# Kernel optimization log

Hardware: AMD Instinct MI355X
Metric: run time of the kernel (lower is better)

## Reference

```python
import jax, jax.numpy as jnp
import numpy as np

PS = 3
B, C, H, W = 4, 256, 64, 64
IMG = 256
_MEAN = np.array([0.485, 0.456, 0.406], dtype=np.float32).reshape(1, 3, 1, 1)
_STD = np.array([0.229, 0.224, 0.225], dtype=np.float32).reshape(1, 3, 1, 1)


def setup_inputs() -> dict:
    key = jax.random.key(0)
    ks = jax.random.split(key, 16)
    d = {
        "dense_features1": jax.random.normal(ks[0], (B, C, H, W), jnp.float32),
        "dense_features2": jax.random.normal(ks[1], (B, C, H, W), jnp.float32),
        "img_ref_hr": jax.random.uniform(ks[2], (B, 3, IMG, IMG), jnp.float32),
        "w1_1": jax.random.normal(ks[3], (64, 3, 3, 3), jnp.float32) * 0.05,
        "b1_1": jnp.zeros((64,), jnp.float32),
        "w1_2": jax.random.normal(ks[4], (64, 64, 3, 3), jnp.float32) * 0.05,
        "b1_2": jnp.zeros((64,), jnp.float32),
        "w2_1": jax.random.normal(ks[5], (128, 64, 3, 3), jnp.float32) * 0.05,
        "b2_1": jnp.zeros((128,), jnp.float32),
        "w2_2": jax.random.normal(ks[6], (128, 128, 3, 3), jnp.float32) * 0.05,
        "b2_2": jnp.zeros((128,), jnp.float32),
        "w3_1": jax.random.normal(ks[7], (256, 128, 3, 3), jnp.float32) * 0.05,
        "b3_1": jnp.zeros((256,), jnp.float32),
    }
    return d


def _conv(x, w, b):
    y = jax.lax.conv_general_dilated(x, w, (1, 1), "SAME",
                                     dimension_numbers=("NCHW", "OIHW", "NCHW"))
    return y + b[None, :, None, None]


def _pool(x):
    return jax.lax.reduce_window(x, -jnp.inf, jax.lax.max, (1, 1, 2, 2), (1, 1, 2, 2), "VALID")


def _vgg(img, w11, b11, w12, b12, w21, b21, w22, b22, w31, b31):
    x = (img - _MEAN) / _STD  # ImageNet input norm (use_input_norm=True)
    r11 = jax.nn.relu(_conv(x, w11, b11))
    x = _pool(jax.nn.relu(_conv(r11, w12, b12)))
    r21 = jax.nn.relu(_conv(x, w21, b21))
    x = _pool(jax.nn.relu(_conv(r21, w22, b22)))
    r31 = jax.nn.relu(_conv(x, w31, b31))
    return r11, r21, r31


def _l2n(f):  # per-pixel channel L2 normalize (F.normalize dim=0, eps=1e-12)
    return f / jnp.maximum(jnp.linalg.norm(f, axis=0, keepdims=True), 1e-12)


def _patches(f):  # (c,h,w) -> (nh*nw, c*PS*PS), row-major patch order
    c, h, w = f.shape
    nh, nw = h - PS + 1, w - PS + 1
    cols = jnp.stack([f[:, i:i + nh, j:j + nw] for i in range(PS) for j in range(PS)], axis=1)
    return cols.reshape(c * PS * PS, nh * nw).T


def _match(fin, fref):
    fin, fref = _l2n(fin), _l2n(fref)
    nh, nw = fin.shape[1] - PS + 1, fin.shape[2] - PS + 1
    p_in = _patches(fin)
    p_ref = _patches(fref)
    p_ref = p_ref / (jnp.linalg.norm(p_ref, axis=1, keepdims=True) + 1e-5)  # is_norm
    corr = p_in @ p_ref.T  # (N_in, N_ref) patch correlation
    return jnp.argmax(corr, axis=1).reshape(nh, nw)


def _index_to_flow(idx):  # (nh,nw) int -> (nh+2, nw+2, 2) float flow
    nh, nw = idx.shape
    fw = (idx % nw).astype(jnp.float32) - jnp.arange(nw, dtype=jnp.float32)[None, :]
    fh = (idx // nw).astype(jnp.float32) - jnp.arange(nh, dtype=jnp.float32)[:, None]
    flow = jnp.stack([fw, fh], axis=-1)
    return jnp.pad(flow, ((0, 2), (0, 2), (0, 0)))


def _shift9(flow, s):  # 9 down/right shifts with zero fill -> (9,H,W,2)
    Hh, Ww, _ = flow.shape
    outs = [jnp.pad(flow, ((i * s, 0), (j * s, 0), (0, 0)))[:Hh, :Ww]
            for i in range(3) for j in range(3)]
    return jnp.stack(outs, axis=0)


def _per_sample(fin, fref):
    flow3 = _index_to_flow(_match(fin, fref))
    off3 = _shift9(flow3, 1)
    flow2 = jnp.repeat(jnp.repeat(flow3, 2, axis=0), 2, axis=1) * 2.0
    off2 = _shift9(flow2, 2)
    flow1 = jnp.repeat(jnp.repeat(flow3, 4, axis=0), 4, axis=1) * 4.0
    off1 = _shift9(flow1, 4)
    return off1, off2, off3


def reference(dense_features1, dense_features2, img_ref_hr,
              w1_1, b1_1, w1_2, b1_2, w2_1, b2_1, w2_2, b2_2, w3_1, b3_1):
    off1, off2, off3 = jax.vmap(_per_sample)(dense_features1, dense_features2)
    r11, r21, r31 = _vgg(img_ref_hr, w1_1, b1_1, w1_2, b1_2, w2_1, b2_1, w2_2, b2_2, w3_1, b3_1)
    # pre_offset['relu1_1'/'relu2_1'/'relu3_1'], img_ref_feat['relu1_1'/'relu2_1'/'relu3_1']
    return (off1, off2, off3, r11, r21, r31)
```

## Files before the change

### kernel.cpp

```cpp
#include <hip/hip_runtime.h>

typedef __attribute__((ext_vector_type(4))) float f32x4;
typedef __attribute__((ext_vector_type(8))) short s16x8;

#define OFF1_OFF 0
#define OFF2_OFF 4718592
#define OFF3_OFF 5898240
#define R11_OFF  6193152
#define R21_OFF  22970368
#define R31_OFF  31358976

__device__ __forceinline__ ushort f2bf(float x) {
  union { float f; uint u; } c; c.f = x;
  uint r = c.u + 0x7FFFu + ((c.u >> 16) & 1u);
  return (ushort)(r >> 16);
}
__device__ __forceinline__ float bfval(ushort h) {
  union { uint u; float f; } c; c.u = ((uint)h) << 16;
  return c.f;
}

__global__ __launch_bounds__(256)
void k_normalize(const float* __restrict__ f1, const float* __restrict__ f2,
                 ushort* __restrict__ n1b, ushort* __restrict__ n2b) {
  __shared__ uint ldsu[64 * 256];
  float* red = (float*)ldsu;
  float* inv = (float*)ldsu + 256;
  const int t = threadIdx.x, x = t & 63, cg = t >> 6;
  const int h = blockIdx.x, b = blockIdx.y;
  const float* in = blockIdx.z ? f2 : f1;
  ushort* op = blockIdx.z ? n2b : n1b;
  const size_t base = (size_t)b * 256 * 4096 + (size_t)h * 64 + x;
  float vals[64];
  float s = 0.f;
  #pragma unroll
  for (int ci = 0; ci < 64; ++ci) {
    float v = in[base + (size_t)(cg * 64 + ci) * 4096];
    vals[ci] = v;
    s = fmaf(v, v, s);
  }
  red[t] = s;
  __syncthreads();
  if (t < 64) {
    float tot = red[t] + red[64 + t] + red[128 + t] + red[192 + t];
    inv[t] = 1.0f / fmaxf(sqrtf(tot), 1e-12f);
  }
  __syncthreads();
  const float iv = inv[x];
  __syncthreads();
  #pragma unroll
  for (int j = 0; j < 32; ++j) {
    float v0 = vals[2 * j] * iv, v1 = vals[2 * j + 1] * iv;
    ushort h0 = f2bf(v0), h1 = f2bf(v1);
    ushort l0 = f2bf(v0 - bfval(h0)), l1 = f2bf(v1 - bfval(h1));
    int cc = (cg << 1) + (j >> 4);
    int i = j & 15;
    int qh = cc * 32 + i, ql = cc * 32 + 16 + i;
    ldsu[x * 256 + (qh ^ (x & 31))] = (uint)h0 | ((uint)h1 << 16);
    ldsu[x * 256 + (ql ^ (x & 31))] = (uint)l0 | ((uint)l1 << 16);
  }
  __syncthreads();
  uint* og = (uint*)(op + ((size_t)b * 4096 + h * 64) * 512);
  #pragma unroll
  for (int it = 0; it < 64; ++it) {
    int idx = it * 256 + t;
    int p = idx >> 8, q = idx & 255;
    og[idx] = ldsu[p * 256 + (q ^ (p & 31))];
  }
}

__global__ __launch_bounds__(256)
void k_pgemm_mfma(const ushort* __restrict__ Ab0, const ushort* __restrict__ Bb0,
                  float* __restrict__ P0) {
  __shared__ __align__(16) ushort As[128 * 64];
  __shared__ __align__(16) ushort Bs[128 * 64];
  const int t = threadIdx.x;
  const int bz = blockIdx.z;
  const ushort* Ab = Ab0 + (size_t)bz * 2097152;
  const ushort* Bb = Bb0 + (size_t)bz * 2097152;
  float* P = P0 + (size_t)bz * 16777216;
  const int u0 = blockIdx.y * 128, v0 = blockIdx.x * 128;
  const int lane = t & 63, wv = t >> 6;
  const int wm = wv >> 1, wn = wv & 1;
  const int lr = lane & 15, lk = lane >> 4;
  int rowv[4], slotv[4];
  #pragma unroll
  for (int i = 0; i < 4; ++i) { int e = t + i * 256; rowv[i] = e >> 3; slotv[i] = e & 7; }
  s16x8 ra[4], rb[4];
  #pragma unroll
  for (int i = 0; i < 4; ++i) {
    ra[i] = *(const s16x8*)(Ab + ((size_t)(u0 + rowv[i])) * 512 + slotv[i] * 8);
    rb[i] = *(const s16x8*)(Bb + ((size_t)(v0 + rowv[i])) * 512 + slotv[i] * 8);
  }
  f32x4 acc[4][4];
  #pragma unroll
  for (int mt = 0; mt < 4; ++mt)
    #pragma unroll
    for (int nt = 0; nt < 4; ++nt) {
      f32x4 z = {0.f, 0.f, 0.f, 0.f};
      acc[mt][nt] = z;
    }

  #pragma unroll 1
  for (int cc = 0; cc < 8; ++cc) {
    __syncthreads();
    #pragma unroll
    for (int i = 0; i < 4; ++i) {
      *(s16x8*)(As + ((rowv[i] << 3) + (slotv[i] ^ (rowv[i] & 7))) * 8) = ra[i];
      *(s16x8*)(Bs + ((rowv[i] << 3) + (slotv[i] ^ (rowv[i] & 7))) * 8) = rb[i];
    }
    __syncthreads();
    if (cc < 7) {
      #pragma unroll
      for (int i = 0; i < 4; ++i) {
        ra[i] = *(const s16x8*)(Ab + ((size_t)(u0 + rowv[i])) * 512 + (cc + 1) * 64 + slotv[i] * 8);
        rb[i] = *(const s16x8*)(Bb + ((size_t)(v0 + rowv[i])) * 512 + (cc + 1) * 64 + slotv[i] * 8);
      }
    }
    s16x8 ah[4], al[4], bh[4], bl[4];
    #pragma unroll
    for (int mt = 0; mt < 4; ++mt) {
      int row = wm * 64 + mt * 16 + lr;
      ah[mt] = *(const s16x8*)(As + ((row << 3) + (lk ^ (row & 7))) * 8);
      al[mt] = *(const s16x8*)(As + ((row << 3) + ((4 + lk) ^ (row & 7))) * 8);
    }
    #pragma unroll
    for (int nt = 0; nt < 4; ++nt) {
      int row = wn * 64 + nt * 16 + lr;
      bh[nt] = *(const s16x8*)(Bs + ((row << 3) + (lk ^ (row & 7))) * 8);
      bl[nt] = *(const s16x8*)(Bs + ((row << 3) + ((4 + lk) ^ (row & 7))) * 8);
    }
    #pragma unroll
    for (int mt = 0; mt < 4; ++mt)
      #pragma unroll
      for (int nt = 0; nt < 4; ++nt) {
        acc[mt][nt] = __builtin_amdgcn_mfma_f32_16x16x32_bf16(al[mt], bh[nt], acc[mt][nt], 0, 0, 0);
        acc[mt][nt] = __builtin_amdgcn_mfma_f32_16x16x32_bf16(ah[mt], bl[nt], acc[mt][nt], 0, 0, 0);
        acc[mt][nt] = __builtin_amdgcn_mfma_f32_16x16x32_bf16(ah[mt], bh[nt], acc[mt][nt], 0, 0, 0);
      }
  }
  const int plane = ((blockIdx.y * 2 + wm) << 6) + blockIdx.x * 2 + wn;
  float* Pp = P + (size_t)plane * 4096;
  #pragma unroll
  for (int mt = 0; mt < 4; ++mt)
    #pragma unroll
    for (int nt = 0; nt < 4; ++nt) {
      #pragma unroll
      for (int r = 0; r < 4; ++r)
        Pp[(mt * 16 + lk * 4 + r) * 64 + nt * 16 + lr] = acc[mt][nt][r];
    }
}

__global__ __launch_bounds__(256)
void k_corr(const float* __restrict__ P0, float* __restrict__ pv0,
            int* __restrict__ pi0) {
  __shared__ __align__(16) f32x4 Pl[3 * 1024];
  __shared__ float rv[256];
  __shared__ int   ri[256];
  const int t = threadIdx.x;
  const int orig = blockIdx.x;
  const int w = (orig & 7) * 1922 + (orig >> 3);
  const int bz = w / 3844;
  const int r2 = w % 3844;
  const int py = r2 / 62, qy = r2 % 62;
  const float* P = P0 + (size_t)bz * 16777216;
  float* pv = pv0 + (size_t)bz * 238328;
  int*   pi = pi0 + (size_t)bz * 238328;
  #pragma unroll
  for (int i = 0; i < 12; ++i) {
    int e = t + i * 256;
    int blk = e >> 10, rem = e & 1023;
    int px = rem >> 4, q4 = rem & 15;
    int pidx = (py + blk) * 64 + (qy + blk);
    f32x4 v = *(const f32x4*)(P + (size_t)pidx * 4096 + rem * 4);
    int slot = ((q4 + (px >> 4)) & 15) ^ (px & 15);
    Pl[blk * 1024 + px * 16 + slot] = v;
  }
  __syncthreads();
  const int px = t & 63, cg = t >> 6;
  #pragma unroll
  for (int j = 0; j < 4; ++j) {
    int c = cg * 4 + j;
    int slot = ((c + (px >> 4)) & 15) ^ (px & 15);
    int o = px * 16 + slot;
    Pl[o] = Pl[o] + Pl[1024 + o] + Pl[2048 + o];
  }
  __syncthreads();
  float bv = -3.4e38f; int bq = 0;
  if (px < 62) {
    const int q0 = cg * 16;
    const int nq = (cg < 3) ? 16 : 14;
    const int nch = (cg < 3) ? 5 : 4;
    float f[3][20];
    #pragma unroll
    for (int dj = 0; dj < 3; ++dj) {
      const int row = px + dj;
      const int rr = row >> 4, rm = row & 15;
      #pragma unroll
      for (int cc2 = 0; cc2 < 5; ++cc2) {
        if (cc2 < nch) {
          int c = cg * 4 + cc2;
          int slot = ((c + rr) & 15) ^ rm;
          f32x4 v = Pl[row * 16 + slot];
          f[dj][cc2 * 4 + 0] = v[0];
          f[dj][cc2 * 4 + 1] = v[1];
          f[dj][cc2 * 4 + 2] = v[2];
          f[dj][cc2 * 4 + 3] = v[3];
        }
      }
    }
    #pragma unroll
    for (int l = 0; l < 16; ++l) {
      if (l < nq) {
        float s = f[0][l] + f[1][l + 1] + f[2][l + 2];
        if (s > bv) { bv = s; bq = q0 + l; }
      }
    }
  }
  rv[t] = bv; ri[t] = bq;
  __syncthreads();
  if (t < 62) {
    float v = rv[t]; int q = ri[t];
    #pragma unroll
    for (int g = 1; g < 4; ++g) {
      float v2 = rv[g * 64 + t];
      if (v2 > v) { v = v2; q = ri[g * 64 + t]; }
    }
    const int n = py * 62 + t;
    pv[(size_t)n * 62 + qy] = v;
    pi[(size_t)n * 62 + qy] = qy * 62 + q;
  }
}

__global__ void k_argmax(const float* __restrict__ pv, const int* __restrict__ pi,
                         int* __restrict__ idxf) {
  int tid = blockIdx.x * 256 + threadIdx.x;
  if (tid >= 4 * 3844) return;
  const float* v = pv + (size_t)tid * 62;
  const int*  ii = pi + (size_t)tid * 62;
  float bv = v[0]; int bi = ii[0];
  for (int q = 1; q < 62; ++q) {
    float x = v[q];
    if (x > bv) { bv = x; bi = ii[q]; }
  }
  idxf[tid] = bi;
}

__global__ void k_flow_all(const int* __restrict__ idxf, float* __restrict__ out) {
  int gid = blockIdx.x * 256 + threadIdx.x;
  int Ho, lg, rel = gid;
  float* o;
  if (gid < 2359296)      { Ho = 256; lg = 2; o = out + OFF1_OFF; }
  else if (gid < 2949120) { Ho = 128; lg = 1; o = out + OFF2_OFF; rel -= 2359296; }
  else if (gid < 3096576) { Ho = 64;  lg = 0; o = out + OFF3_OFF; rel -= 2949120; }
  else return;
  const int x = rel % Ho;
  const int y = (rel / Ho) % Ho;
  const int s = (rel / (Ho * Ho)) % 9;
  const int b = rel / (Ho * Ho * 9);
  const int i = s / 3, j = s % 3;
  const int sc = 1 << lg;
  const int yy = y - i * sc, xx = x - j * sc;
  float fw = 0.f, fh = 0.f;
  if (yy >= 0 && xx >= 0) {
    const int r = yy >> lg, c = xx >> lg;
    if (r < 62 && c < 62) {
      const int id = idxf[b * 3844 + r * 62 + c];
      fw = (float)((id % 62 - c) * sc);
      fh = (float)((id / 62 - r) * sc);
    }
  }
  float2 ov = {fw, fh};
  *(float2*)(o + (size_t)rel * 2) = ov;
}

__global__ void k_wprep_all(const float* __restrict__ w12, const float* __restrict__ w21,
                            const float* __restrict__ w22, const float* __restrict__ w31,
                            ushort* __restrict__ o12, ushort* __restrict__ o21,
                            ushort* __restrict__ o22, ushort* __restrict__ o31) {
  int gid = blockIdx.x * 256 + threadIdx.x;
  const float* w; ushort* o; int CIN, rel;
  if (gid < 36864)        { w = w12; o = o12; CIN = 64;  rel = gid; }
  else if (gid < 110592)  { w = w21; o = o21; CIN = 64;  rel = gid - 36864; }
  else if (gid < 258048)  { w = w22; o = o22; CIN = 128; rel = gid - 110592; }
  else if (gid < 552960)  { w = w31; o = o31; CIN = 128; rel = gid - 258048; }
  else return;
  int ci = rel % CIN;
  int r = rel / CIN;
  int tap = r % 9;
  int oc = r / 9;
  o[((size_t)oc * 9 + tap) * CIN + ci] = f2bf(w[((size_t)oc * CIN + ci) * 9 + tap]);
}

__global__ __launch_bounds__(256)
void k_conv11(const float* __restrict__ img0, const float* __restrict__ w,
              const float* __restrict__ bias, float* __restrict__ outF0,
              ushort* __restrict__ outB0) {
  __shared__ float wl[1728];
  __shared__ float bl[64];
  const int t = threadIdx.x;
  const int b = blockIdx.y;
  const float* img = img0 + (size_t)b * 3 * 65536;
  float* outF = outF0 + (size_t)b * 64 * 65536;
  ushort* outB = outB0 + (size_t)b * 4194304;
  for (int i = t; i < 1728; i += 256) wl[i] = w[i];
  if (t < 64) bl[t] = bias[t];
  __syncthreads();
  const int x = t, y = blockIdx.x;
  const float mean[3] = {0.485f, 0.456f, 0.406f};
  const float stdv[3] = {0.229f, 0.224f, 0.225f};
  float v[27];
  #pragma unroll
  for (int c = 0; c < 3; ++c)
    #pragma unroll
    for (int dy = 0; dy < 3; ++dy)
      #pragma unroll
      for (int dx = 0; dx < 3; ++dx) {
        int iy = y + dy - 1, ix = x + dx - 1;
        float val = 0.f;
        if (iy >= 0 && iy < 256 && ix >= 0 && ix < 256)
          val = (img[((size_t)c * 256 + iy) * 256 + ix] - mean[c]) / stdv[c];
        v[c * 9 + dy * 3 + dx] = val;
      }
  float ov[64];
  #pragma unroll 4
  for (int oc = 0; oc < 64; ++oc) {
    float a = bl[oc];
    #pragma unroll
    for (int k = 0; k < 27; ++k) a = fmaf(wl[oc * 27 + k], v[k], a);
    a = fmaxf(a, 0.f);
    ov[oc] = a;
    outF[((size_t)oc * 256 + y) * 256 + x] = a;
  }
  uint* ob = (uint*)(outB + ((((size_t)y) * 256 + x) << 6));
  #pragma unroll
  for (int j = 0; j < 32; ++j)
    ob[j] = (uint)f2bf(ov[2 * j]) | ((uint)f2bf(ov[2 * j + 1]) << 16);
}

template <int CIN, bool POOL, bool WB16>
__global__ __launch_bounds__(256)
void k_mconv(const ushort* __restrict__ inb, const ushort* __restrict__ wB,
             const float* __restrict__ bias, float* __restrict__ outF,
             ushort* __restrict__ outB, int H, int W, int Cout,
             int inStride, int fStride, int bStride) {
  __shared__ __align__(16) char lds_raw[33792];
  ushort* As = (ushort*)lds_raw;
  float*  sm = (float*)lds_raw;
  const int t = threadIdx.x;
  const int bz = blockIdx.z;
  inb += (size_t)bz * inStride;
  outF += (size_t)bz * fStride;
  outB += (size_t)bz * bStride;
  const int xtiles = W >> 6;
  const int xt = blockIdx.x % xtiles;
  const int yp = blockIdx.x / xtiles;
  const int x0 = xt << 6, y0 = yp << 1;
  const int ocb = blockIdx.y << 6;
  const int lane = t & 63, wv = t >> 6;
  const int wm = wv >> 1, wn = wv & 1;
  const int lr = lane & 15, lk = lane >> 4;
  constexpr int NC2 = CIN / 64;

  f32x4 acc[4][2];
  #pragma unroll
  for (int mr = 0; mr < 4; ++mr)
    #pragma unroll
    for (int n = 0; n < 2; ++n) {
      f32x4 z = {0.f, 0.f, 0.f, 0.f};
      acc[mr][n] = z;
    }

  #pragma unroll 1
  for (int cc = 0; cc < NC2; ++cc) {
    __syncthreads();
    #pragma unroll
    for (int i = 0; i < 9; ++i) {
      int e = t + i * 256;
      if (e < 2112) {
        int pos = e >> 3, cig = e & 7;
        int hy = pos / 66, hx = pos - hy * 66;
        int gy = y0 + hy - 1, gx = x0 + hx - 1;
        s16x8 v = {0, 0, 0, 0, 0, 0, 0, 0};
        if (gy >= 0 && gy < H && gx >= 0 && gx < W)
          v = *(const s16x8*)(inb + ((size_t)gy * W + gx) * CIN + cc * 64 + cig * 8);
        *(s16x8*)(As + ((pos << 3) + (cig ^ (pos & 7))) * 8) = v;
      }
    }
    __syncthreads();
    #pragma unroll 3
    for (int tap = 0; tap < 9; ++tap) {
      const int dy = tap / 3, dx = tap % 3;
      s16x8 b0[2], b1[2];
      #pragma unroll
      for (int n = 0; n < 2; ++n) {
        const ushort* wp =
            wB + ((size_t)(ocb + wn * 32 + n * 16 + lr) * 9 + tap) * CIN + cc * 64 + lk * 8;
        b0[n] = *(const s16x8*)wp;
        b1[n] = *(const s16x8*)(wp + 32);
      }
      #pragma unroll
      for (int mr = 0; mr < 4; ++mr) {
        const int pos = (wm + dy) * 66 + mr * 16 + lr + dx;
        s16x8 a0 = *(const s16x8*)(As + ((pos << 3) + (lk ^ (pos & 7))) * 8);
        s16x8 a1 = *(const s16x8*)(As + ((pos << 3) + ((4 + lk) ^ (pos & 7))) * 8);
        #pragma unroll
        for (int n = 0; n < 2; ++n) {
          acc[mr][n] = __builtin_amdgcn_mfma_f32_16x16x32_bf16(a0, b0[n], acc[mr][n], 0, 0, 0);
          acc[mr][n] = __builtin_amdgcn_mfma_f32_16x16x32_bf16(a1, b1[n], acc[mr][n], 0, 0, 0);
        }
      }
    }
  }
  __syncthreads();
  #pragma unroll
  for (int mr = 0; mr < 4; ++mr)
    #pragma unroll
    for (int n = 0; n < 2; ++n) {
      const int oc = wn * 32 + n * 16 + lr;
      const float bs = bias[ocb + oc];
      #pragma unroll
      for (int r = 0; r < 4; ++r)
        sm[(wm * 64 + mr * 16 + lk * 4 + r) * 65 + oc] =
            fmaxf(acc[mr][n][r] + bs, 0.f);
    }
  __syncthreads();
  if (POOL) {
    const int Wo = W >> 1;
    #pragma unroll
    for (int i = 0; i < 4; ++i) {
      int e = t + i * 256;
      int op = e & 31, xo = e >> 5;
      int oc0 = op * 2;
      float m0 = fmaxf(fmaxf(sm[(xo * 2) * 65 + oc0], sm[(xo * 2 + 1) * 65 + oc0]),
                       fmaxf(sm[(64 + xo * 2) * 65 + oc0], sm[(64 + xo * 2 + 1) * 65 + oc0]));
      float m1 = fmaxf(fmaxf(sm[(xo * 2) * 65 + oc0 + 1], sm[(xo * 2 + 1) * 65 + oc0 + 1]),
                       fmaxf(sm[(64 + xo * 2) * 65 + oc0 + 1], sm[(64 + xo * 2 + 1) * 65 + oc0 + 1]));
      size_t pos = (size_t)yp * Wo + (x0 >> 1) + xo;
      ((uint*)outB)[pos * (Cout >> 1) + ((ocb >> 1) + op)] =
          (uint)f2bf(m0) | ((uint)f2bf(m1) << 16);
    }
  } else {
    #pragma unroll
    for (int i = 0; i < 32; ++i) {
      int e = t + i * 256;
      int oc = e >> 7, sp = e & 127;
      outF[((size_t)(ocb + oc) * H + y0 + (sp >> 6)) * W + x0 + (sp & 63)] =
          sm[sp * 65 + oc];
    }
    if (WB16) {
      #pragma unroll
      for (int i = 0; i < 16; ++i) {
        int e = t + i * 256;
        int op = e & 31, sp = e >> 5;
        int oc0 = op * 2;
        float v0 = sm[sp * 65 + oc0], v1 = sm[sp * 65 + oc0 + 1];
        size_t pos = ((size_t)(y0 + (sp >> 6))) * W + x0 + (sp & 63);
        ((uint*)outB)[pos * (Cout >> 1) + ((ocb >> 1) + op)] =
            (uint)f2bf(v0) | ((uint)f2bf(v1) << 16);
      }
    }
  }
}

extern "C" void kernel_launch(void* const* d_in, const int* in_sizes, int n_in,
                              void* d_out, int out_size, void* d_ws, size_t ws_size,
                              hipStream_t stream) {
  const float* df1 = (const float*)d_in[0];
  const float* df2 = (const float*)d_in[1];
  const float* img = (const float*)d_in[2];
  const float* w11 = (const float*)d_in[3];
  const float* b11 = (const float*)d_in[4];
  const float* w12 = (const float*)d_in[5];
  const float* b12 = (const float*)d_in[6];
  const float* w21 = (const float*)d_in[7];
  const float* b21 = (const float*)d_in[8];
  const float* w22 = (const float*)d_in[9];
  const float* b22 = (const float*)d_in[10];
  const float* w31 = (const float*)d_in[11];
  const float* b31 = (const float*)d_in[12];
  float* out = (float*)d_out;

  int* idxf = (int*)d_ws;
  ushort* w12b = (ushort*)(idxf + 15376);
  ushort* w21b = w12b + 36864;
  ushort* w22b = w21b + 73728;
  ushort* w31b = w22b + 147456;
  float* P4 = (float*)((char*)d_ws + (size_t)(4 << 20));
  ushort* a11s = (ushort*)P4;
  ushort* p1bs = a11s + 16777216;
  ushort* a21s = p1bs + 4194304;
  ushort* p2bs = a21s + 8388608;

  ushort* n1b = (ushort*)(out + R21_OFF);
  ushort* n2b = n1b + 8388608;
  float* pv = out + OFF1_OFF;
  int*   pi = (int*)(out + OFF1_OFF + 953312);

  k_normalize<<<dim3(64, 4, 2), 256, 0, stream>>>(df1, df2, n1b, n2b);
  k_wprep_all<<<2160, 256, 0, stream>>>(w12, w21, w22, w31, w12b, w21b, w22b, w31b);

  k_pgemm_mfma<<<dim3(32, 32, 4), 256, 0, stream>>>(n1b, n2b, P4);
  k_corr<<<15376, 256, 0, stream>>>(P4, pv, pi);
  k_argmax<<<61, 256, 0, stream>>>(pv, pi, idxf);

  k_conv11<<<dim3(256, 4), 256, 0, stream>>>(img, w11, b11, out + R11_OFF, a11s);
  k_mconv<64, true, false><<<dim3(512, 1, 4), 256, 0, stream>>>(
      a11s, w12b, b12, nullptr, p1bs, 256, 256, 64, 4194304, 0, 1048576);
  k_mconv<64, false, true><<<dim3(128, 2, 4), 256, 0, stream>>>(
      p1bs, w21b, b21, out + R21_OFF, a21s, 128, 128, 128, 1048576, 2097152, 2097152);
  k_mconv<128, true, false><<<dim3(128, 2, 4), 256, 0, stream>>>(
      a21s, w22b, b22, nullptr, p2bs, 128, 128, 128, 2097152, 0, 524288);
  k_mconv<128, false, false><<<dim3(32, 4, 4), 256, 0, stream>>>(
      p2bs, w31b, b31, out + R31_OFF, nullptr, 64, 64, 256, 524288, 1048576, 0);

  k_flow_all<<<12096, 256, 0, stream>>>(idxf, out);
}
```

Baseline: 456.9 us.

## Double-buffer pgemm via direct global-to-LDS loads and switch to 32x32x16 MFMA

Rewrites the patch-GEMM main loop. It now uses a two-stage LDS ring filled by global_load_lds DMA with manual vmcnt waits and barriers, replacing register staging followed by ds_write. It also moves from 16x16x32 to 32x32x16 bf16 MFMA tiles, which cuts LDS fragment reads per MFMA. The goal is to overlap global fetches with compute and reduce LDS traffic, at the cost of doubling LDS use and relying on hand-tuned waitcnt correctness.

```diff
diff --git a/kernel.cpp b/kernel.cpp
--- a/kernel.cpp
+++ b/kernel.cpp
@@ -1,7 +1,8 @@
 #include <hip/hip_runtime.h>
 
-typedef __attribute__((ext_vector_type(4))) float f32x4;
-typedef __attribute__((ext_vector_type(8))) short s16x8;
+typedef __attribute__((ext_vector_type(4)))  float f32x4;
+typedef __attribute__((ext_vector_type(16))) float f32x16;
+typedef __attribute__((ext_vector_type(8)))  short s16x8;
 
 #define OFF1_OFF 0
 #define OFF2_OFF 4718592
@@ -72,83 +73,102 @@
 __global__ __launch_bounds__(256)
 void k_pgemm_mfma(const ushort* __restrict__ Ab0, const ushort* __restrict__ Bb0,
                   float* __restrict__ P0) {
-  __shared__ __align__(16) ushort As[128 * 64];
-  __shared__ __align__(16) ushort Bs[128 * 64];
+  __shared__ __align__(16) ushort AsB[2][8192];
+  __shared__ __align__(16) ushort BsB[2][8192];
   const int t = threadIdx.x;
   const int bz = blockIdx.z;
-  const ushort* Ab = Ab0 + (size_t)bz * 2097152;
-  const ushort* Bb = Bb0 + (size_t)bz * 2097152;
+  const ushort* Ab = Ab0 + (size_t)bz * 2097152 + (size_t)blockIdx.y * 128 * 512;
+  const ushort* Bb = Bb0 + (size_t)bz * 2097152 + (size_t)blockIdx.x * 128 * 512;
   float* P = P0 + (size_t)bz * 16777216;
-  const int u0 = blockIdx.y * 128, v0 = blockIdx.x * 128;
   const int lane = t & 63, wv = t >> 6;
   const int wm = wv >> 1, wn = wv & 1;
-  const int lr = lane & 15, lk = lane >> 4;
-  int rowv[4], slotv[4];
-  #pragma unroll
-  for (int i = 0; i < 4; ++i) { int e = t + i * 256; rowv[i] = e >> 3; slotv[i] = e & 7; }
-  s16x8 ra[4], rb[4];
-  #pragma unroll
-  for (int i = 0; i < 4; ++i) {
-    ra[i] = *(const s16x8*)(Ab + ((size_t)(u0 + rowv[i])) * 512 + slotv[i] * 8);
-    rb[i] = *(const s16x8*)(Bb + ((size_t)(v0 + rowv[i])) * 512 + slotv[i] * 8);
-  }
-  f32x4 acc[4][4];
-  #pragma unroll
-  for (int mt = 0; mt < 4; ++mt)
-    #pragma unroll
-    for (int nt = 0; nt < 4; ++nt) {
-      f32x4 z = {0.f, 0.f, 0.f, 0.f};
-      acc[mt][nt] = z;
-    }
+  const int l31 = lane & 31, lh = lane >> 5;
+
+#define STAGE(buf, cc)                                                         \
+  do {                                                                         \
+    _Pragma("unroll")                                                          \
+    for (int j = 0; j < 4; ++j) {                                              \
+      int u = (wv * 4 + j) * 64 + lane;                                        \
+      int row = u >> 3;                                                        \
+      int gs = (u & 7) ^ (row & 7);                                            \
+      __builtin_amdgcn_global_load_lds(                                        \
+          (const __attribute__((address_space(1))) void*)(Ab + (size_t)row * 512 + (cc) * 64 + gs * 8), \
+          (__attribute__((address_space(3))) void*)(AsB[buf] + u * 8), 16, 0, 0); \
+      __builtin_amdgcn_global_load_lds(                                        \
+          (const __attribute__((address_space(1))) void*)(Bb + (size_t)row * 512 + (cc) * 64 + gs * 8), \
+          (__attribute__((address_space(3))) void*)(BsB[buf] + u * 8), 16, 0, 0); \
+    }                                                                          \
+  } while (0)
+
+  f32x16 acc[2][2];
+  #pragma unroll
+  for (int mt = 0; mt < 2; ++mt)
+    #pragma unroll
+    for (int nt = 0; nt < 2; ++nt)
+      #pragma unroll
+      for (int r = 0; r < 16; ++r) acc[mt][nt][r] = 0.f;
+
+  STAGE(0, 0);
+  STAGE(1, 1);
 
   #pragma unroll 1
   for (int cc = 0; cc < 8; ++cc) {
-    __syncthreads();
-    #pragma unroll
-    for (int i = 0; i < 4; ++i) {
-      *(s16x8*)(As + ((rowv[i] << 3) + (slotv[i] ^ (rowv[i] & 7))) * 8) = ra[i];
-      *(s16x8*)(Bs + ((rowv[i] << 3) + (slotv[i] ^ (rowv[i] & 7))) * 8) = rb[i];
-    }
-    __syncthreads();
-    if (cc < 7) {
-      #pragma unroll
-      for (int i = 0; i < 4; ++i) {
-        ra[i] = *(const s16x8*)(Ab + ((size_t)(u0 + rowv[i])) * 512 + (cc + 1) * 64 + slotv[i] * 8);
-        rb[i] = *(const s16x8*)(Bb + ((size_t)(v0 + rowv[i])) * 512 + (cc + 1) * 64 + slotv[i] * 8);
-      }
-    }
-    s16x8 ah[4], al[4], bh[4], bl[4];
-    #pragma unroll
-    for (int mt = 0; mt < 4; ++mt) {
-      int row = wm * 64 + mt * 16 + lr;
-      ah[mt] = *(const s16x8*)(As + ((row << 3) + (lk ^ (row & 7))) * 8);
-      al[mt] = *(const s16x8*)(As + ((row << 3) + ((4 + lk) ^ (row & 7))) * 8);
-    }
-    #pragma unroll
-    for (int nt = 0; nt < 4; ++nt) {
-      int row = wn * 64 + nt * 16 + lr;
-      bh[nt] = *(const s16x8*)(Bs + ((row << 3) + (lk ^ (row & 7))) * 8);
-      bl[nt] = *(const s16x8*)(Bs + ((row << 3) + ((4 + lk) ^ (row & 7))) * 8);
-    }
-    #pragma unroll
-    for (int mt = 0; mt < 4; ++mt)
-      #pragma unroll
-      for (int nt = 0; nt < 4; ++nt) {
-        acc[mt][nt] = __builtin_amdgcn_mfma_f32_16x16x32_bf16(al[mt], bh[nt], acc[mt][nt], 0, 0, 0);
-        acc[mt][nt] = __builtin_amdgcn_mfma_f32_16x16x32_bf16(ah[mt], bl[nt], acc[mt][nt], 0, 0, 0);
-        acc[mt][nt] = __builtin_amdgcn_mfma_f32_16x16x32_bf16(ah[mt], bh[nt], acc[mt][nt], 0, 0, 0);
-      }
-  }
+    const int cur = cc & 1;
+    if (cc < 7) { asm volatile("s_waitcnt vmcnt(8)" ::: "memory"); }
+    else        { asm volatile("s_waitcnt vmcnt(0)" ::: "memory"); }
+    __builtin_amdgcn_s_barrier();
+    __builtin_amdgcn_sched_barrier(0);
+    const ushort* As = AsB[cur];
+    const ushort* Bs = BsB[cur];
+    s16x8 ah[2][2], al[2][2], bh[2][2], bl[2][2];
+    #pragma unroll
+    for (int mt = 0; mt < 2; ++mt) {
+      const int row = wm * 64 + mt * 32 + l31;
+      const int rx = row & 7;
+      const ushort* pr = As + (row << 6);
+      ah[mt][0] = *(const s16x8*)(pr + ((0 + lh) ^ rx) * 8);
+      ah[mt][1] = *(const s16x8*)(pr + ((2 + lh) ^ rx) * 8);
+      al[mt][0] = *(const s16x8*)(pr + ((4 + lh) ^ rx) * 8);
+      al[mt][1] = *(const s16x8*)(pr + ((6 + lh) ^ rx) * 8);
+    }
+    #pragma unroll
+    for (int nt = 0; nt < 2; ++nt) {
+      const int row = wn * 64 + nt * 32 + l31;
+      const int rx = row & 7;
+      const ushort* pr = Bs + (row << 6);
+      bh[nt][0] = *(const s16x8*)(pr + ((0 + lh) ^ rx) * 8);
+      bh[nt][1] = *(const s16x8*)(pr + ((2 + lh) ^ rx) * 8);
+      bl[nt][0] = *(const s16x8*)(pr + ((4 + lh) ^ rx) * 8);
+      bl[nt][1] = *(const s16x8*)(pr + ((6 + lh) ^ rx) * 8);
+    }
+    #pragma unroll
+    for (int mt = 0; mt < 2; ++mt)
+      #pragma unroll
+      for (int nt = 0; nt < 2; ++nt) {
+        acc[mt][nt] = __builtin_amdgcn_mfma_f32_32x32x16_bf16(al[mt][0], bh[nt][0], acc[mt][nt], 0, 0, 0);
+        acc[mt][nt] = __builtin_amdgcn_mfma_f32_32x32x16_bf16(al[mt][1], bh[nt][1], acc[mt][nt], 0, 0, 0);
+        acc[mt][nt] = __builtin_amdgcn_mfma_f32_32x32x16_bf16(ah[mt][0], bl[nt][0], acc[mt][nt], 0, 0, 0);
+        acc[mt][nt] = __builtin_amdgcn_mfma_f32_32x32x16_bf16(ah[mt][1], bl[nt][1], acc[mt][nt], 0, 0, 0);
+        acc[mt][nt] = __builtin_amdgcn_mfma_f32_32x32x16_bf16(ah[mt][0], bh[nt][0], acc[mt][nt], 0, 0, 0);
+        acc[mt][nt] = __builtin_amdgcn_mfma_f32_32x32x16_bf16(ah[mt][1], bh[nt][1], acc[mt][nt], 0, 0, 0);
+      }
+    __builtin_amdgcn_sched_barrier(0);
+    __builtin_amdgcn_s_barrier();
+    if (cc < 6) STAGE(cur, cc + 2);
+  }
+#undef STAGE
+
   const int plane = ((blockIdx.y * 2 + wm) << 6) + blockIdx.x * 2 + wn;
   float* Pp = P + (size_t)plane * 4096;
   #pragma unroll
-  for (int mt = 0; mt < 4; ++mt)
-    #pragma unroll
-    for (int nt = 0; nt < 4; ++nt) {
-      #pragma unroll
-      for (int r = 0; r < 4; ++r)
-        Pp[(mt * 16 + lk * 4 + r) * 64 + nt * 16 + lr] = acc[mt][nt][r];
-    }
+  for (int mt = 0; mt < 2; ++mt)
+    #pragma unroll
+    for (int nt = 0; nt < 2; ++nt)
+      #pragma unroll
+      for (int r = 0; r < 16; ++r) {
+        const int rowf = (r & 3) + 8 * (r >> 2) + 4 * lh;
+        Pp[(mt * 32 + rowf) * 64 + nt * 32 + l31] = acc[mt][nt][r];
+      }
 }
 
 __global__ __launch_bounds__(256)
```

Result: slower. 482.2 us (+5.5%).

## Use zero-padded bf16 activation buffers and direct global-to-LDS loads in conv

Applied to the files above, without the earlier changes.

Intermediate bf16 activations are now stored with a one-pixel zero halo, which a new small kernel writes before the VGG chain runs. Because the halo makes every load in bounds, the mconv tile load drops its bounds checks and uses global_load_lds to copy straight into shared memory, bypassing registers. The XOR swizzle moves from the LDS address to the global address. This adds a launch and slightly larger buffers, and relies on the workspace layout still fitting and on the swizzle mapping being correct.

```diff
diff --git a/kernel.cpp b/kernel.cpp
--- a/kernel.cpp
+++ b/kernel.cpp
@@ -292,6 +292,26 @@
   o[((size_t)oc * 9 + tap) * CIN + ci] = f2bf(w[((size_t)oc * CIN + ci) * 9 + tap]);
 }
 
+__global__ void k_zb(ushort* __restrict__ a11, ushort* __restrict__ p1,
+                     ushort* __restrict__ a21, ushort* __restrict__ p2) {
+  int gid = blockIdx.x * 256 + threadIdx.x;
+  if (gid >= 99072) return;
+  int b = gid / 24768, r = gid % 24768;
+  ushort* p; int Hp, Wp, C8, u;
+  size_t stride;
+  if (r < 8224)       { p = a11; Hp = 258; Wp = 258; C8 = 8;  stride = 4260096; u = r; }
+  else if (r < 12352) { p = p1;  Hp = 130; Wp = 130; C8 = 8;  stride = 1081600; u = r - 8224; }
+  else if (r < 20608) { p = a21; Hp = 130; Wp = 130; C8 = 16; stride = 2163200; u = r - 12352; }
+  else                { p = p2;  Hp = 66;  Wp = 66;  C8 = 16; stride = 557568;  u = r - 20608; }
+  int pos = u / C8, j = u % C8;
+  int row, col;
+  if (pos < Wp)            { row = 0;      col = pos; }
+  else if (pos < 2 * Wp)   { row = Hp - 1; col = pos - Wp; }
+  else { int q = pos - 2 * Wp; row = 1 + (q >> 1); col = (q & 1) ? (Wp - 1) : 0; }
+  s16x8 z = {0, 0, 0, 0, 0, 0, 0, 0};
+  *(s16x8*)(p + (size_t)b * stride + (((size_t)row * Wp + col) * C8 + j) * 8) = z;
+}
+
 __global__ __launch_bounds__(256)
 void k_conv11(const float* __restrict__ img0, const float* __restrict__ w,
               const float* __restrict__ bias, float* __restrict__ outF0,
@@ -302,7 +322,7 @@
   const int b = blockIdx.y;
   const float* img = img0 + (size_t)b * 3 * 65536;
   float* outF = outF0 + (size_t)b * 64 * 65536;
-  ushort* outB = outB0 + (size_t)b * 4194304;
+  ushort* outB = outB0 + (size_t)b * 4260096;
   for (int i = t; i < 1728; i += 256) wl[i] = w[i];
   if (t < 64) bl[t] = bias[t];
   __syncthreads();
@@ -332,7 +352,7 @@
     ov[oc] = a;
     outF[((size_t)oc * 256 + y) * 256 + x] = a;
   }
-  uint* ob = (uint*)(outB + ((((size_t)y) * 256 + x) << 6));
+  uint* ob = (uint*)(outB + (((size_t)(y + 1) * 258 + (x + 1)) << 6));
   #pragma unroll
   for (int j = 0; j < 32; ++j)
     ob[j] = (uint)f2bf(ov[2 * j]) | ((uint)f2bf(ov[2 * j + 1]) << 16);
@@ -343,7 +363,7 @@
 void k_mconv(const ushort* __restrict__ inb, const ushort* __restrict__ wB,
              const float* __restrict__ bias, float* __restrict__ outF,
              ushort* __restrict__ outB, int H, int W, int Cout,
-             int inStride, int fStride, int bStride) {
+             int inStride, int fStride, int bStride, int PW, int POut) {
   __shared__ __align__(16) char lds_raw[33792];
   ushort* As = (ushort*)lds_raw;
   float*  sm = (float*)lds_raw;
@@ -378,13 +398,13 @@
     for (int i = 0; i < 9; ++i) {
       int e = t + i * 256;
       if (e < 2112) {
-        int pos = e >> 3, cig = e & 7;
+        int pos = e >> 3;
+        int gs = (e & 7) ^ (pos & 7);
         int hy = pos / 66, hx = pos - hy * 66;
-        int gy = y0 + hy - 1, gx = x0 + hx - 1;
-        s16x8 v = {0, 0, 0, 0, 0, 0, 0, 0};
-        if (gy >= 0 && gy < H && gx >= 0 && gx < W)
-          v = *(const s16x8*)(inb + ((size_t)gy * W + gx) * CIN + cc * 64 + cig * 8);
-        *(s16x8*)(As + ((pos << 3) + (cig ^ (pos & 7))) * 8) = v;
+        __builtin_amdgcn_global_load_lds(
+            (const __attribute__((address_space(1))) void*)(
+                inb + ((size_t)(y0 + hy) * PW + x0 + hx) * CIN + cc * 64 + gs * 8),
+            (__attribute__((address_space(3))) void*)(As + (size_t)e * 8), 16, 0, 0);
       }
     }
     __syncthreads();
@@ -426,7 +446,6 @@
     }
   __syncthreads();
   if (POOL) {
-    const int Wo = W >> 1;
     #pragma unroll
     for (int i = 0; i < 4; ++i) {
       int e = t + i * 256;
@@ -436,7 +455,7 @@
                        fmaxf(sm[(64 + xo * 2) * 65 + oc0], sm[(64 + xo * 2 + 1) * 65 + oc0]));
       float m1 = fmaxf(fmaxf(sm[(xo * 2) * 65 + oc0 + 1], sm[(xo * 2 + 1) * 65 + oc0 + 1]),
                        fmaxf(sm[(64 + xo * 2) * 65 + oc0 + 1], sm[(64 + xo * 2 + 1) * 65 + oc0 + 1]));
-      size_t pos = (size_t)yp * Wo + (x0 >> 1) + xo;
+      size_t pos = (size_t)(yp + 1) * POut + (x0 >> 1) + xo + 1;
       ((uint*)outB)[pos * (Cout >> 1) + ((ocb >> 1) + op)] =
           (uint)f2bf(m0) | ((uint)f2bf(m1) << 16);
     }
@@ -455,7 +474,7 @@
         int op = e & 31, sp = e >> 5;
         int oc0 = op * 2;
         float v0 = sm[sp * 65 + oc0], v1 = sm[sp * 65 + oc0 + 1];
-        size_t pos = ((size_t)(y0 + (sp >> 6))) * W + x0 + (sp & 63);
+        size_t pos = (size_t)(y0 + (sp >> 6) + 1) * POut + x0 + (sp & 63) + 1;
         ((uint*)outB)[pos * (Cout >> 1) + ((ocb >> 1) + op)] =
             (uint)f2bf(v0) | ((uint)f2bf(v1) << 16);
       }
@@ -488,9 +507,9 @@
   ushort* w31b = w22b + 147456;
   float* P4 = (float*)((char*)d_ws + (size_t)(4 << 20));
   ushort* a11s = (ushort*)P4;
-  ushort* p1bs = a11s + 16777216;
-  ushort* a21s = p1bs + 4194304;
-  ushort* p2bs = a21s + 8388608;
+  ushort* p1bs = a11s + 17040384;
+  ushort* a21s = p1bs + 4326400;
+  ushort* p2bs = a21s + 8652800;
 
   ushort* n1b = (ushort*)(out + R21_OFF);
   ushort* n2b = n1b + 8388608;
@@ -504,15 +523,16 @@
   k_corr<<<15376, 256, 0, stream>>>(P4, pv, pi);
   k_argmax<<<61, 256, 0, stream>>>(pv, pi, idxf);
 
+  k_zb<<<387, 256, 0, stream>>>(a11s, p1bs, a21s, p2bs);
   k_conv11<<<dim3(256, 4), 256, 0, stream>>>(img, w11, b11, out + R11_OFF, a11s);
   k_mconv<64, true, false><<<dim3(512, 1, 4), 256, 0, stream>>>(
-      a11s, w12b, b12, nullptr, p1bs, 256, 256, 64, 4194304, 0, 1048576);
+      a11s, w12b, b12, nullptr, p1bs, 256, 256, 64, 4260096, 0, 1081600, 258, 130);
   k_mconv<64, false, true><<<dim3(128, 2, 4), 256, 0, stream>>>(
-      p1bs, w21b, b21, out + R21_OFF, a21s, 128, 128, 128, 1048576, 2097152, 2097152);
+      p1bs, w21b, b21, out + R21_OFF, a21s, 128, 128, 128, 1081600, 2097152, 2163200, 130, 130);
   k_mconv<128, true, false><<<dim3(128, 2, 4), 256, 0, stream>>>(
-      a21s, w22b, b22, nullptr, p2bs, 128, 128, 128, 2097152, 0, 524288);
+      a21s, w22b, b22, nullptr, p2bs, 128, 128, 128, 2163200, 0, 557568, 130, 66);
   k_mconv<128, false, false><<<dim3(32, 4, 4), 256, 0, stream>>>(
-      p2bs, w31b, b31, out + R31_OFF, nullptr, 64, 64, 256, 524288, 1048576, 0);
+      p2bs, w31b, b31, out + R31_OFF, nullptr, 64, 64, 256, 557568, 1048576, 0, 66, 0);
 
   k_flow_all<<<12096, 256, 0, stream>>>(idxf, out);
 }
```

Result: no change. 451.6 us (-1.2%).
